# Kernel tuning notes

Hardware: AMD Instinct MI355X
Metric: run time of the kernel (lower is better)

## Reference

```python
import jax, jax.numpy as jnp
import numpy as np
import math

E, K = 8, 4
IN, OUT = 768, 768
B, S = 16, 512

def _nearest_factors(n):
    r = int(math.sqrt(n))
    while n % r != 0:
        r -= 1
    r = max(r, 1)
    return r, n // r

D1, D2 = _nearest_factors(IN)      # 24, 32
DO1, DO2 = _nearest_factors(OUT)   # 24, 32

def _cv_squared(v):
    v = v.astype(jnp.float32)
    return jnp.var(v, ddof=1) / (jnp.mean(v) ** 2 + 1e-10)

def setup_inputs() -> dict:
    key = jax.random.key(0)
    ks = jax.random.split(key, 8)
    eye = lambda d: jnp.broadcast_to(jnp.eye(d, dtype=jnp.float32), (E, d, d))
    return {
        "x": jax.random.normal(ks[0], (B, S, IN), jnp.float32),
        "w_gate": 0.02 * jax.random.normal(ks[1], (IN, E), jnp.float32),
        "weight": 0.02 * jax.random.normal(ks[2], (E, OUT, IN), jnp.float32),
        "res_weight": 0.02 * jax.random.normal(ks[3], (OUT, IN), jnp.float32),
        "curve1_in": eye(D1) + 0.01 * jax.random.normal(ks[4], (E, D1, D1), jnp.float32),
        "curve2_in": eye(D2) + 0.01 * jax.random.normal(ks[5], (E, D2, D2), jnp.float32),
        "curve1_out": eye(DO1) + 0.01 * jax.random.normal(ks[6], (E, DO1, DO1), jnp.float32),
        "curve2_out": eye(DO2) + 0.01 * jax.random.normal(ks[7], (E, DO2, DO2), jnp.float32),
    }

def reference(x, w_gate, weight, res_weight, curve1_in, curve2_in, curve1_out, curve2_out):
    b = x.shape[0]
    # ---- noisy_top_k_gating (eval mode: clean logits, no noise) ----
    xm = x.mean(-2)                         # [B, IN]
    logits = xm @ w_gate                    # [B, E]
    top_vals, top_idx = jax.lax.top_k(logits, min(K + 1, E))
    tk_vals = top_vals[:, :K]
    tk_idx = top_idx[:, :K]
    tk_gates = jax.nn.softmax(tk_vals, axis=1)
    gates = jnp.zeros_like(logits).at[jnp.arange(b)[:, None], tk_idx].set(tk_gates)
    load = (gates > 0).sum(0)               # eval: gates_to_load
    importance = gates.sum(0)
    loss = 0.01 * (_cv_squared(importance) + _cv_squared(load))
    # ---- curve-factor expert weight composition (k*2 >= n_experts branch) ----
    rtw = (weight - res_weight).reshape(E, DO1, DO2, D1, D2)
    rtw = jnp.einsum('bij,bjklm->biklm', curve1_out, rtw)
    rtw = jnp.einsum('bik,bjklm->bjilm', curve2_out, rtw)
    rtw = jnp.einsum('bil,bjklm->bjkim', curve1_in, rtw)
    rtw = jnp.einsum('bim,bjklm->bjkli', curve2_in, rtw)
    rtw = rtw.reshape(E, OUT, IN)
    # dropout p=0.1 is identity in eval mode
    expert_weights = res_weight + 0.9 * jnp.sum(rtw[None] * gates[:, :, None, None], axis=1)  # [B, OUT, IN]
    y = jnp.einsum('bsj,bkj->bsk', x, expert_weights)  # [B, S, OUT]
    return y, loss
```

## Files before the change

kernel.cpp:

```cpp
#include <hip/hip_runtime.h>
#include <hip/hip_bf16.h>

typedef unsigned short u16;
typedef __attribute__((ext_vector_type(8))) short bf16x8;
typedef __attribute__((ext_vector_type(4))) float f32x4;

#define NE 8
#define NTOPK 4
#define NIN 768
#define NOUT 768
#define NB 16
#define NS 512
#define YSZ (NB * NS * NOUT)
#define EWN (NOUT * NIN)

#define OFF_PART  0u
#define OFF_GATES 1048576u
#define OFF_XBF   1049088u
#define OFF_WD    13632000u
#define OFF_T1T   23069184u
#define OFF_RTW   32506368u
#define OFF_EW    41943552u

__device__ __forceinline__ u16 f2bf(float f) {
  union { float f; unsigned u; } v; v.f = f;
  unsigned r = v.u + 0x7fffu + ((v.u >> 16) & 1u);
  return (u16)(r >> 16);
}
__device__ __forceinline__ float bf2f(u16 h) {
  union { unsigned u; float f; } v; v.u = ((unsigned)h) << 16;
  return v.f;
}
__device__ __forceinline__ unsigned cvt2(float a, float b) {
  unsigned r;
  asm("v_cvt_pk_bf16_f32 %0, %1, %2" : "=v"(r) : "v"(a), "v"(b));
  return r;
}

__device__ __forceinline__ void gload16(const void* g, void* l) {
  __builtin_amdgcn_global_load_lds(
      (const __attribute__((address_space(1))) unsigned int*)g,
      (__attribute__((address_space(3))) unsigned int*)l, 16, 0, 0);
}

__device__ __forceinline__ void storeC(float* p, float v) { *p = v; }
__device__ __forceinline__ void storeC(u16* p, float v) { *p = f2bf(v); }

__global__ __launch_bounds__(192) void k_xm(const float* __restrict__ x,
                                            float* __restrict__ part,
                                            u16* __restrict__ xbf) {
  int b = blockIdx.x >> 4;
  int sc = blockIdx.x & 15;
  int t = threadIdx.x;
  int c = t * 4;
  float a0 = 0.f, a1 = 0.f, a2 = 0.f, a3 = 0.f;
  int s0 = sc * 32;
  for (int s = s0; s < s0 + 32; ++s) {
    size_t ro = ((size_t)(b * NS + s)) * NIN;
    float4 v = *(const float4*)(x + ro + c);
    a0 += v.x; a1 += v.y; a2 += v.z; a3 += v.w;
    ushort4 o;
    o.x = f2bf(v.x); o.y = f2bf(v.y); o.z = f2bf(v.z); o.w = f2bf(v.w);
    *(ushort4*)(xbf + ro + c) = o;
  }
  float4 pv; pv.x = a0; pv.y = a1; pv.z = a2; pv.w = a3;
  *(float4*)(part + (size_t)(b * 16 + sc) * NIN + c) = pv;
}

__global__ __launch_bounds__(256) void k_logits(const float* __restrict__ part,
                                                const float* __restrict__ w_gate,
                                                float* __restrict__ gates_out) {
  int b = blockIdx.x;
  int tid = threadIdx.x;
  float p[NE] = {0.f, 0.f, 0.f, 0.f, 0.f, 0.f, 0.f, 0.f};
  for (int i = tid; i < NIN; i += 256) {
    float s = 0.f;
#pragma unroll
    for (int sc = 0; sc < 16; ++sc) s += part[(size_t)(b * 16 + sc) * NIN + i];
    float xmv = s * (1.0f / (float)NS);
#pragma unroll
    for (int e = 0; e < NE; ++e) p[e] += xmv * w_gate[i * NE + e];
  }
  __shared__ float red[4 * NE];
#pragma unroll
  for (int e = 0; e < NE; ++e) {
    float v = p[e];
    for (int off = 32; off; off >>= 1) v += __shfl_down(v, off);
    if ((tid & 63) == 0) red[(tid >> 6) * NE + e] = v;
  }
  __syncthreads();
  if (tid == 0) {
    float v[NE]; bool used[NE];
    for (int e = 0; e < NE; ++e) {
      v[e] = red[e] + red[NE + e] + red[2 * NE + e] + red[3 * NE + e];
      used[e] = false;
    }
    int idxs[NTOPK]; float vals[NTOPK];
    for (int t = 0; t < NTOPK; ++t) {
      int best = 0; float bv = -3.4e38f;
      for (int e = 0; e < NE; ++e)
        if (!used[e] && v[e] > bv) { bv = v[e]; best = e; }
      used[best] = true; idxs[t] = best; vals[t] = bv;
    }
    float m = vals[0];
    float ex[NTOPK]; float se = 0.f;
    for (int t = 0; t < NTOPK; ++t) { ex[t] = expf(vals[t] - m); se += ex[t]; }
    float g[NE];
    for (int e = 0; e < NE; ++e) g[e] = 0.f;
    for (int t = 0; t < NTOPK; ++t) g[idxs[t]] = ex[t] / se;
    for (int e = 0; e < NE; ++e) gates_out[b * NE + e] = g[e];
  }
}

__global__ __launch_bounds__(256) void k_wd(const float* __restrict__ w,
                                            const float* __restrict__ res,
                                            u16* __restrict__ Wd) {
  int e = blockIdx.y;
  size_t base = (size_t)blockIdx.x * 2048 + threadIdx.x * 8;
  float4 wa = *(const float4*)(w + (size_t)e * EWN + base);
  float4 wb = *(const float4*)(w + (size_t)e * EWN + base + 4);
  float4 ra = *(const float4*)(res + base);
  float4 rb = *(const float4*)(res + base + 4);
  bf16x8 o;
  o[0] = (short)f2bf(wa.x - ra.x); o[1] = (short)f2bf(wa.y - ra.y);
  o[2] = (short)f2bf(wa.z - ra.z); o[3] = (short)f2bf(wa.w - ra.w);
  o[4] = (short)f2bf(wb.x - rb.x); o[5] = (short)f2bf(wb.y - rb.y);
  o[6] = (short)f2bf(wb.z - rb.z); o[7] = (short)f2bf(wb.w - rb.w);
  *(bf16x8*)(Wd + (size_t)e * EWN + base) = o;
}

template <typename CT>
__global__ __launch_bounds__(256) void gemm_kron(const float* __restrict__ c1,
                                                 const float* __restrict__ c2,
                                                 const u16* __restrict__ B,
                                                 CT* __restrict__ C) {
  __shared__ u16 lB[2][128 * 32];
  const int tid = threadIdx.x;
  const int lane = tid & 63;
  const int w = tid >> 6;
  const int wr = w >> 1, wc = w & 1;
  const int fr = lane & 15;
  const int kq = lane >> 4;

  const int nwg = gridDim.x;
  const int swz = (blockIdx.x & 7) * (nwg >> 3) + (blockIdx.x >> 3);
  const int mb = swz % 12;
  const int nb = (swz / 12) % 6;
  const int e = swz / 72;

  const int m0 = mb * 64, n0 = nb * 128;
  const u16* Bb = B + (size_t)e * EWN;
  const float* c1b = c1 + e * 24 * 24;
  const float* c2b = c2 + e * 32 * 32;

  const int r1a = (m0 >> 5) + wr;
  float c2r[2][8];
  {
    const float* p0 = c2b + fr * 32 + kq * 8;
    const float* p1 = c2b + (16 + fr) * 32 + kq * 8;
#pragma unroll
    for (int j = 0; j < 8; ++j) { c2r[0][j] = p0[j]; c2r[1][j] = p1[j]; }
  }

  const int ob1 = (w * 2) * 1024 + lane * 16;
  const int ob2 = ob1 + 1024;
  const int rowB1 = ob1 >> 6, colB1 = ob1 & 63;
  const int rowB2 = ob2 >> 6, colB2 = ob2 & 63;

  auto STAGE = [&](int k0, int s) {
    gload16((const char*)Bb + ((size_t)(n0 + rowB1) * NIN + k0) * 2 + colB1,
            (char*)&lB[s][0] + ob1);
    gload16((const char*)Bb + ((size_t)(n0 + rowB2) * NIN + k0) * 2 + colB2,
            (char*)&lB[s][0] + ob2);
  };

  f32x4 acc[2][4] = {};
  STAGE(0, 0);
  __syncthreads();
  int cur = 0;
  for (int k0 = 0; k0 < NIN; k0 += 32) {
    if (k0 + 32 < NIN) STAGE(k0 + 32, cur ^ 1);
    const int l0 = k0 >> 5;
    const float ca = c1b[r1a * 24 + l0];
    bf16x8 aF[2], bF[4];
#pragma unroll
    for (int m = 0; m < 2; ++m) {
      union { unsigned u[4]; bf16x8 v; } pk;
      pk.u[0] = cvt2(ca * c2r[m][0], ca * c2r[m][1]);
      pk.u[1] = cvt2(ca * c2r[m][2], ca * c2r[m][3]);
      pk.u[2] = cvt2(ca * c2r[m][4], ca * c2r[m][5]);
      pk.u[3] = cvt2(ca * c2r[m][6], ca * c2r[m][7]);
      aF[m] = pk.v;
    }
#pragma unroll
    for (int n = 0; n < 4; ++n)
      bF[n] = *(const bf16x8*)&lB[cur][(wc * 64 + n * 16 + fr) * 32 + kq * 8];
#pragma unroll
    for (int m = 0; m < 2; ++m)
#pragma unroll
      for (int n = 0; n < 4; ++n)
        acc[m][n] = __builtin_amdgcn_mfma_f32_16x16x32_bf16(aF[m], bF[n], acc[m][n], 0, 0, 0);
    __syncthreads();
    cur ^= 1;
  }

  CT* Cb = C + (size_t)e * EWN;
#pragma unroll
  for (int m = 0; m < 2; ++m) {
    int rb = m0 + wr * 32 + m * 16 + kq * 4;
#pragma unroll
    for (int n = 0; n < 4; ++n) {
      int col = n0 + wc * 64 + n * 16 + fr;
#pragma unroll
      for (int r = 0; r < 4; ++r)
        storeC(&Cb[(size_t)(rb + r) * NIN + col], acc[m][n][r]);
    }
  }
}

__global__ __launch_bounds__(256) void gemm_main(const u16* __restrict__ A,
                                                 const u16* __restrict__ Bw,
                                                 float* __restrict__ C) {
  __shared__ u16 lA[2][64 * 32];
  __shared__ u16 lB[2][128 * 32];
  const int tid = threadIdx.x;
  const int lane = tid & 63;
  const int w = tid >> 6;
  const int wr = w >> 1, wc = w & 1;
  const int fr = lane & 15;
  const int kq = lane >> 4;

  const int nwg = gridDim.x;
  const int swz = (blockIdx.x & 7) * (nwg >> 3) + (blockIdx.x >> 3);
  const int mb = swz % 8;
  const int nb = (swz / 8) % 6;
  const int b = swz / 48;

  const int m0 = mb * 64, n0 = nb * 128;
  const u16* Ab = A + (size_t)b * NS * NIN;
  const u16* Bb = Bw + (size_t)b * EWN;

  const int obA = tid * 16;
  const int rowA = obA >> 6, colA = obA & 63;
  const int obB1 = (w * 2) * 1024 + lane * 16;
  const int obB2 = obB1 + 1024;
  const int rowB1 = obB1 >> 6, colB1 = obB1 & 63;
  const int rowB2 = obB2 >> 6, colB2 = obB2 & 63;

  auto STAGE = [&](int k0, int s) {
    gload16((const char*)Ab + ((size_t)(m0 + rowA) * NIN + k0) * 2 + colA,
            (char*)&lA[s][0] + obA);
    gload16((const char*)Bb + ((size_t)(n0 + rowB1) * NIN + k0) * 2 + colB1,
            (char*)&lB[s][0] + obB1);
    gload16((const char*)Bb + ((size_t)(n0 + rowB2) * NIN + k0) * 2 + colB2,
            (char*)&lB[s][0] + obB2);
  };

  f32x4 acc[2][4] = {};
  STAGE(0, 0);
  __syncthreads();
  int cur = 0;
  for (int k0 = 0; k0 < NIN; k0 += 32) {
    if (k0 + 32 < NIN) STAGE(k0 + 32, cur ^ 1);
    bf16x8 aF[2], bF[4];
#pragma unroll
    for (int m = 0; m < 2; ++m)
      aF[m] = *(const bf16x8*)&lA[cur][(wr * 32 + m * 16 + fr) * 32 + kq * 8];
#pragma unroll
    for (int n = 0; n < 4; ++n)
      bF[n] = *(const bf16x8*)&lB[cur][(wc * 64 + n * 16 + fr) * 32 + kq * 8];
#pragma unroll
    for (int m = 0; m < 2; ++m)
#pragma unroll
      for (int n = 0; n < 4; ++n)
        acc[m][n] = __builtin_amdgcn_mfma_f32_16x16x32_bf16(aF[m], bF[n], acc[m][n], 0, 0, 0);
    __syncthreads();
    cur ^= 1;
  }

  float* Cb = C + (size_t)b * NS * NOUT;
#pragma unroll
  for (int m = 0; m < 2; ++m) {
    int rb = m0 + wr * 32 + m * 16 + kq * 4;
#pragma unroll
    for (int n = 0; n < 4; ++n) {
      int col = n0 + wc * 64 + n * 16 + fr;
#pragma unroll
      for (int r = 0; r < 4; ++r)
        Cb[(size_t)(rb + r) * NOUT + col] = acc[m][n][r];
    }
  }
}

__global__ __launch_bounds__(256) void k_combine(const u16* __restrict__ rtwb,
                                                 const float* __restrict__ res,
                                                 const float* __restrict__ g,
                                                 u16* __restrict__ ew,
                                                 float* __restrict__ loss_out) {
  __shared__ float gs[NB * NE];
  int tid = threadIdx.x;
  if (tid < NB * NE) gs[tid] = 0.9f * g[tid];
  __syncthreads();
  if (blockIdx.x == 0 && tid == 0) {
    float imp[NE], ld[NE];
    for (int e = 0; e < NE; ++e) {
      float si = 0.f, sl = 0.f;
      for (int b = 0; b < NB; ++b) {
        float gg = g[b * NE + e];
        si += gg; sl += (gg > 0.f) ? 1.f : 0.f;
      }
      imp[e] = si; ld[e] = sl;
    }
    float loss = 0.f;
    for (int which = 0; which < 2; ++which) {
      const float* a = which ? ld : imp;
      float mean = 0.f;
      for (int e = 0; e < NE; ++e) mean += a[e];
      mean *= (1.0f / NE);
      float var = 0.f;
      for (int e = 0; e < NE; ++e) { float d = a[e] - mean; var += d * d; }
      var *= (1.0f / (NE - 1));
      loss += var / (mean * mean + 1e-10f);
    }
    loss_out[0] = 0.01f * loss;
  }
  size_t base = ((size_t)blockIdx.x * 256 + tid) * 8;
  float rv[NE][8];
#pragma unroll
  for (int e = 0; e < NE; ++e) {
    bf16x8 v = *(const bf16x8*)(rtwb + (size_t)e * EWN + base);
#pragma unroll
    for (int j = 0; j < 8; ++j) rv[e][j] = bf2f((u16)v[j]);
  }
  float r8[8];
  {
    float4 ra = *(const float4*)(res + base);
    float4 rb = *(const float4*)(res + base + 4);
    r8[0] = ra.x; r8[1] = ra.y; r8[2] = ra.z; r8[3] = ra.w;
    r8[4] = rb.x; r8[5] = rb.y; r8[6] = rb.z; r8[7] = rb.w;
  }
  for (int b = 0; b < NB; ++b) {
    float a[8];
#pragma unroll
    for (int j = 0; j < 8; ++j) a[j] = r8[j];
#pragma unroll
    for (int e = 0; e < NE; ++e) {
      float gg = gs[b * NE + e];
#pragma unroll
      for (int j = 0; j < 8; ++j) a[j] += gg * rv[e][j];
    }
    bf16x8 o;
#pragma unroll
    for (int j = 0; j < 8; ++j) o[j] = (short)f2bf(a[j]);
    *(bf16x8*)(ew + (size_t)b * EWN + base) = o;
  }
}

extern "C" void kernel_launch(void* const* d_in, const int* in_sizes, int n_in,
                              void* d_out, int out_size, void* d_ws, size_t ws_size,
                              hipStream_t stream) {
  const float* x = (const float*)d_in[0];
  const float* w_gate = (const float*)d_in[1];
  const float* weight = (const float*)d_in[2];
  const float* res_w = (const float*)d_in[3];
  const float* c1i = (const float*)d_in[4];
  const float* c2i = (const float*)d_in[5];
  const float* c1o = (const float*)d_in[6];
  const float* c2o = (const float*)d_in[7];

  char* ws = (char*)d_ws;
  float* part = (float*)(ws + OFF_PART);
  float* gates = (float*)(ws + OFF_GATES);
  u16* xbf = (u16*)(ws + OFF_XBF);
  u16* Wd = (u16*)(ws + OFF_WD);
  u16* T1t = (u16*)(ws + OFF_T1T);
  u16* rtwb = (u16*)(ws + OFF_RTW);
  u16* ew = (u16*)(ws + OFF_EW);

  float* y = (float*)d_out;
  float* loss = y + YSZ;

  k_xm<<<dim3(256), 192, 0, stream>>>(x, part, xbf);
  k_logits<<<dim3(NB), 256, 0, stream>>>(part, w_gate, gates);
  k_wd<<<dim3(288, 8), 256, 0, stream>>>(weight, res_w, Wd);
  gemm_kron<u16><<<dim3(576), 256, 0, stream>>>(c1i, c2i, Wd, T1t);
  gemm_kron<u16><<<dim3(576), 256, 0, stream>>>(c1o, c2o, T1t, rtwb);
  k_combine<<<dim3(288), 256, 0, stream>>>(rtwb, res_w, gates, ew, loss);
  gemm_main<<<dim3(768), 256, 0, stream>>>(xbf, ew, y);
}
```

Measured before the change: 89.21 us.

## Deepen GEMM LDS pipeline to four stages and merge xm/wd kernels

Both GEMM kernels move from double buffering to a 4-deep LDS ring with three tiles in flight. Each step now waits with an explicit partial vmcnt before the barrier instead of a full __syncthreads, so global loads overlap more with the MFMA work. The x-mean/bf16 cast kernel and the weight-difference kernel are fused into one launch, removing a kernel boundary. In exchange LDS use doubles, which may cut occupancy, and the hand-written waitcnt counts must exactly match the number of loads issued per stage.

```diff
diff --git a/kernel.cpp b/kernel.cpp
--- a/kernel.cpp
+++ b/kernel.cpp
@@ -22,6 +22,9 @@
 #define OFF_RTW   32506368u
 #define OFF_EW    41943552u
 
+#define PRE_BAR(N) asm volatile("s_waitcnt vmcnt(" #N ")\n\ts_barrier" ::: "memory")
+#define POST_BAR() asm volatile("s_waitcnt lgkmcnt(0)\n\ts_barrier" ::: "memory")
+
 __device__ __forceinline__ u16 f2bf(float f) {
   union { float f; unsigned u; } v; v.f = f;
   unsigned r = v.u + 0x7fffu + ((v.u >> 16) & 1u);
@@ -46,25 +49,48 @@
 __device__ __forceinline__ void storeC(float* p, float v) { *p = v; }
 __device__ __forceinline__ void storeC(u16* p, float v) { *p = f2bf(v); }
 
-__global__ __launch_bounds__(192) void k_xm(const float* __restrict__ x,
-                                            float* __restrict__ part,
-                                            u16* __restrict__ xbf) {
-  int b = blockIdx.x >> 4;
-  int sc = blockIdx.x & 15;
-  int t = threadIdx.x;
-  int c = t * 4;
-  float a0 = 0.f, a1 = 0.f, a2 = 0.f, a3 = 0.f;
-  int s0 = sc * 32;
-  for (int s = s0; s < s0 + 32; ++s) {
-    size_t ro = ((size_t)(b * NS + s)) * NIN;
-    float4 v = *(const float4*)(x + ro + c);
-    a0 += v.x; a1 += v.y; a2 += v.z; a3 += v.w;
-    ushort4 o;
-    o.x = f2bf(v.x); o.y = f2bf(v.y); o.z = f2bf(v.z); o.w = f2bf(v.w);
-    *(ushort4*)(xbf + ro + c) = o;
-  }
-  float4 pv; pv.x = a0; pv.y = a1; pv.z = a2; pv.w = a3;
-  *(float4*)(part + (size_t)(b * 16 + sc) * NIN + c) = pv;
+__global__ __launch_bounds__(256) void k_xm_wd(const float* __restrict__ x,
+                                               float* __restrict__ part,
+                                               u16* __restrict__ xbf,
+                                               const float* __restrict__ w,
+                                               const float* __restrict__ res,
+                                               u16* __restrict__ Wd) {
+  int bid = blockIdx.x;
+  if (bid < 256) {
+    int t = threadIdx.x;
+    if (t < 192) {
+      int b = bid >> 4;
+      int sc = bid & 15;
+      int c = t * 4;
+      float a0 = 0.f, a1 = 0.f, a2 = 0.f, a3 = 0.f;
+      int s0 = sc * 32;
+      for (int s = s0; s < s0 + 32; ++s) {
+        size_t ro = ((size_t)(b * NS + s)) * NIN;
+        float4 v = *(const float4*)(x + ro + c);
+        a0 += v.x; a1 += v.y; a2 += v.z; a3 += v.w;
+        ushort4 o;
+        o.x = f2bf(v.x); o.y = f2bf(v.y); o.z = f2bf(v.z); o.w = f2bf(v.w);
+        *(ushort4*)(xbf + ro + c) = o;
+      }
+      float4 pv; pv.x = a0; pv.y = a1; pv.z = a2; pv.w = a3;
+      *(float4*)(part + (size_t)(b * 16 + sc) * NIN + c) = pv;
+    }
+  } else {
+    int b2 = bid - 256;
+    int e = b2 / 288;
+    int blk = b2 % 288;
+    size_t base = (size_t)blk * 2048 + threadIdx.x * 8;
+    float4 wa = *(const float4*)(w + (size_t)e * EWN + base);
+    float4 wb = *(const float4*)(w + (size_t)e * EWN + base + 4);
+    float4 ra = *(const float4*)(res + base);
+    float4 rb = *(const float4*)(res + base + 4);
+    bf16x8 o;
+    o[0] = (short)f2bf(wa.x - ra.x); o[1] = (short)f2bf(wa.y - ra.y);
+    o[2] = (short)f2bf(wa.z - ra.z); o[3] = (short)f2bf(wa.w - ra.w);
+    o[4] = (short)f2bf(wb.x - rb.x); o[5] = (short)f2bf(wb.y - rb.y);
+    o[6] = (short)f2bf(wb.z - rb.z); o[7] = (short)f2bf(wb.w - rb.w);
+    *(bf16x8*)(Wd + (size_t)e * EWN + base) = o;
+  }
 }
 
 __global__ __launch_bounds__(256) void k_logits(const float* __restrict__ part,
@@ -112,29 +138,12 @@
   }
 }
 
-__global__ __launch_bounds__(256) void k_wd(const float* __restrict__ w,
-                                            const float* __restrict__ res,
-                                            u16* __restrict__ Wd) {
-  int e = blockIdx.y;
-  size_t base = (size_t)blockIdx.x * 2048 + threadIdx.x * 8;
-  float4 wa = *(const float4*)(w + (size_t)e * EWN + base);
-  float4 wb = *(const float4*)(w + (size_t)e * EWN + base + 4);
-  float4 ra = *(const float4*)(res + base);
-  float4 rb = *(const float4*)(res + base + 4);
-  bf16x8 o;
-  o[0] = (short)f2bf(wa.x - ra.x); o[1] = (short)f2bf(wa.y - ra.y);
-  o[2] = (short)f2bf(wa.z - ra.z); o[3] = (short)f2bf(wa.w - ra.w);
-  o[4] = (short)f2bf(wb.x - rb.x); o[5] = (short)f2bf(wb.y - rb.y);
-  o[6] = (short)f2bf(wb.z - rb.z); o[7] = (short)f2bf(wb.w - rb.w);
-  *(bf16x8*)(Wd + (size_t)e * EWN + base) = o;
-}
-
 template <typename CT>
 __global__ __launch_bounds__(256) void gemm_kron(const float* __restrict__ c1,
                                                  const float* __restrict__ c2,
                                                  const u16* __restrict__ B,
                                                  CT* __restrict__ C) {
-  __shared__ u16 lB[2][128 * 32];
+  __shared__ u16 lB[4][128 * 32];
   const int tid = threadIdx.x;
   const int lane = tid & 63;
   const int w = tid >> 6;
@@ -142,8 +151,7 @@
   const int fr = lane & 15;
   const int kq = lane >> 4;
 
-  const int nwg = gridDim.x;
-  const int swz = (blockIdx.x & 7) * (nwg >> 3) + (blockIdx.x >> 3);
+  const int swz = (blockIdx.x & 7) * 72 + (blockIdx.x >> 3);
   const int mb = swz % 12;
   const int nb = (swz / 12) % 6;
   const int e = swz / 72;
@@ -167,7 +175,8 @@
   const int rowB1 = ob1 >> 6, colB1 = ob1 & 63;
   const int rowB2 = ob2 >> 6, colB2 = ob2 & 63;
 
-  auto STAGE = [&](int k0, int s) {
+  auto STAGE = [&](int t, int s) {
+    int k0 = t * 32;
     gload16((const char*)Bb + ((size_t)(n0 + rowB1) * NIN + k0) * 2 + colB1,
             (char*)&lB[s][0] + ob1);
     gload16((const char*)Bb + ((size_t)(n0 + rowB2) * NIN + k0) * 2 + colB2,
@@ -175,13 +184,9 @@
   };
 
   f32x4 acc[2][4] = {};
-  STAGE(0, 0);
-  __syncthreads();
-  int cur = 0;
-  for (int k0 = 0; k0 < NIN; k0 += 32) {
-    if (k0 + 32 < NIN) STAGE(k0 + 32, cur ^ 1);
-    const int l0 = k0 >> 5;
-    const float ca = c1b[r1a * 24 + l0];
+
+  auto COMPUTE = [&](int t, int s) {
+    const float ca = c1b[r1a * 24 + t];
     bf16x8 aF[2], bF[4];
 #pragma unroll
     for (int m = 0; m < 2; ++m) {
@@ -194,15 +199,24 @@
     }
 #pragma unroll
     for (int n = 0; n < 4; ++n)
-      bF[n] = *(const bf16x8*)&lB[cur][(wc * 64 + n * 16 + fr) * 32 + kq * 8];
+      bF[n] = *(const bf16x8*)&lB[s][(wc * 64 + n * 16 + fr) * 32 + kq * 8];
 #pragma unroll
     for (int m = 0; m < 2; ++m)
 #pragma unroll
       for (int n = 0; n < 4; ++n)
         acc[m][n] = __builtin_amdgcn_mfma_f32_16x16x32_bf16(aF[m], bF[n], acc[m][n], 0, 0, 0);
-    __syncthreads();
-    cur ^= 1;
-  }
+  };
+
+  STAGE(0, 0); STAGE(1, 1); STAGE(2, 2);
+  for (int t = 0; t < 21; ++t) {
+    STAGE(t + 3, (t + 3) & 3);
+    PRE_BAR(6);
+    COMPUTE(t, t & 3);
+    POST_BAR();
+  }
+  PRE_BAR(4);  COMPUTE(21, 1);  POST_BAR();
+  PRE_BAR(2);  COMPUTE(22, 2);  POST_BAR();
+  PRE_BAR(0);  COMPUTE(23, 3);
 
   CT* Cb = C + (size_t)e * EWN;
 #pragma unroll
@@ -221,8 +235,8 @@
 __global__ __launch_bounds__(256) void gemm_main(const u16* __restrict__ A,
                                                  const u16* __restrict__ Bw,
                                                  float* __restrict__ C) {
-  __shared__ u16 lA[2][64 * 32];
-  __shared__ u16 lB[2][128 * 32];
+  __shared__ u16 lA[4][64 * 32];
+  __shared__ u16 lB[4][128 * 32];
   const int tid = threadIdx.x;
   const int lane = tid & 63;
   const int w = tid >> 6;
@@ -230,8 +244,7 @@
   const int fr = lane & 15;
   const int kq = lane >> 4;
 
-  const int nwg = gridDim.x;
-  const int swz = (blockIdx.x & 7) * (nwg >> 3) + (blockIdx.x >> 3);
+  const int swz = (blockIdx.x & 7) * 96 + (blockIdx.x >> 3);
   const int mb = swz % 8;
   const int nb = (swz / 8) % 6;
   const int b = swz / 48;
@@ -247,7 +260,8 @@
   const int rowB1 = obB1 >> 6, colB1 = obB1 & 63;
   const int rowB2 = obB2 >> 6, colB2 = obB2 & 63;
 
-  auto STAGE = [&](int k0, int s) {
+  auto STAGE = [&](int t, int s) {
+    int k0 = t * 32;
     gload16((const char*)Ab + ((size_t)(m0 + rowA) * NIN + k0) * 2 + colA,
             (char*)&lA[s][0] + obA);
     gload16((const char*)Bb + ((size_t)(n0 + rowB1) * NIN + k0) * 2 + colB1,
@@ -257,26 +271,32 @@
   };
 
   f32x4 acc[2][4] = {};
-  STAGE(0, 0);
-  __syncthreads();
-  int cur = 0;
-  for (int k0 = 0; k0 < NIN; k0 += 32) {
-    if (k0 + 32 < NIN) STAGE(k0 + 32, cur ^ 1);
+
+  auto COMPUTE = [&](int s) {
     bf16x8 aF[2], bF[4];
 #pragma unroll
     for (int m = 0; m < 2; ++m)
-      aF[m] = *(const bf16x8*)&lA[cur][(wr * 32 + m * 16 + fr) * 32 + kq * 8];
+      aF[m] = *(const bf16x8*)&lA[s][(wr * 32 + m * 16 + fr) * 32 + kq * 8];
 #pragma unroll
     for (int n = 0; n < 4; ++n)
-      bF[n] = *(const bf16x8*)&lB[cur][(wc * 64 + n * 16 + fr) * 32 + kq * 8];
+      bF[n] = *(const bf16x8*)&lB[s][(wc * 64 + n * 16 + fr) * 32 + kq * 8];
 #pragma unroll
     for (int m = 0; m < 2; ++m)
 #pragma unroll
       for (int n = 0; n < 4; ++n)
         acc[m][n] = __builtin_amdgcn_mfma_f32_16x16x32_bf16(aF[m], bF[n], acc[m][n], 0, 0, 0);
-    __syncthreads();
-    cur ^= 1;
-  }
+  };
+
+  STAGE(0, 0); STAGE(1, 1); STAGE(2, 2);
+  for (int t = 0; t < 21; ++t) {
+    STAGE(t + 3, (t + 3) & 3);
+    PRE_BAR(9);
+    COMPUTE(t & 3);
+    POST_BAR();
+  }
+  PRE_BAR(6);  COMPUTE(1);  POST_BAR();
+  PRE_BAR(3);  COMPUTE(2);  POST_BAR();
+  PRE_BAR(0);  COMPUTE(3);
 
   float* Cb = C + (size_t)b * NS * NOUT;
 #pragma unroll
@@ -380,9 +400,8 @@
   float* y = (float*)d_out;
   float* loss = y + YSZ;
 
-  k_xm<<<dim3(256), 192, 0, stream>>>(x, part, xbf);
+  k_xm_wd<<<dim3(2560), 256, 0, stream>>>(x, part, xbf, weight, res_w, Wd);
   k_logits<<<dim3(NB), 256, 0, stream>>>(part, w_gate, gates);
-  k_wd<<<dim3(288, 8), 256, 0, stream>>>(weight, res_w, Wd);
   gemm_kron<u16><<<dim3(576), 256, 0, stream>>>(c1i, c2i, Wd, T1t);
   gemm_kron<u16><<<dim3(576), 256, 0, stream>>>(c1o, c2o, T1t, rtwb);
   k_combine<<<dim3(288), 256, 0, stream>>>(rtwb, res_w, gates, ew, loss);
```

After: 89.19 us. No clear change (-0.0%).
